# Performance work log

Hardware: AMD Instinct MI355X
Metric: run time of the kernel (lower is better)

## Reference

```python
import jax, jax.numpy as jnp
import numpy as np

N_NODES = 100000
N_EDGES = 3200000
HID = 64


def setup_inputs() -> dict:
    key = jax.random.key(0)
    ks = jax.random.split(key, 20)
    x = jax.random.normal(ks[0], (N_NODES, 3), dtype=jnp.float32)
    edge_index = jax.random.randint(ks[1], (2, N_EDGES), 0, N_NODES, dtype=jnp.int32)

    def glorot(k, fan_in, fan_out):
        s = jnp.sqrt(6.0 / (fan_in + fan_out))
        return jax.random.uniform(k, (fan_in, fan_out), jnp.float32, -s, s)

    W_in = glorot(ks[2], 3, HID)
    b_in = jnp.zeros((HID,), jnp.float32)
    W_hid = jnp.stack([glorot(ks[3 + i], HID, HID) for i in range(6)])  # [6,64,64]
    b_hid = jnp.zeros((6, HID), jnp.float32)
    W_out = glorot(ks[10], HID, 6)
    b_out = jnp.zeros((6,), jnp.float32)
    return {"x": x, "edge_index": edge_index, "W_in": W_in, "b_in": b_in,
            "W_hid": W_hid, "b_hid": b_hid, "W_out": W_out, "b_out": b_out}


def _gcn_layer(x, W, b, src, dst, norm):
    # PyG GCNConv: h = x @ W; out[dst] += norm * h[src]; out += b
    h = x @ W
    msg = h[src] * norm[:, None]            # [E+N, F]
    agg = jax.ops.segment_sum(msg, dst, num_segments=N_NODES)
    return agg + b


def reference(x, edge_index, W_in, b_in, W_hid, b_hid, W_out, b_out):
    # Add self-loops and symmetric normalization (computed once, shared by all layers)
    loops = jnp.arange(N_NODES, dtype=edge_index.dtype)
    src = jnp.concatenate([edge_index[0], loops])
    dst = jnp.concatenate([edge_index[1], loops])
    deg = jax.ops.segment_sum(jnp.ones_like(dst, dtype=x.dtype), dst, num_segments=N_NODES)
    dinv = jnp.where(deg > 0, jax.lax.rsqrt(deg), 0.0)
    norm = dinv[src] * dinv[dst]            # [E+N]

    h = jax.nn.relu(_gcn_layer(x, W_in, b_in, src, dst, norm))
    for i in range(6):
        h = jax.nn.relu(_gcn_layer(h, W_hid[i], b_hid[i], src, dst, norm))
    # dropout p=0.25 with train=False -> identity (eval mode)
    out = _gcn_layer(h, W_out, b_out, src, dst, norm)
    return jax.nn.sigmoid(out)
```

## Files before the change

kernel.cpp:

```cpp
#include <hip/hip_runtime.h>
#include <hip/hip_fp16.h>
#include <math.h>

#define MAXBKT 512


__global__ __launch_bounds__(256) void k_bcount(const int* __restrict__ dstA,
                                                int E, int N, int nbkt, int* bucketCnt) {
    __shared__ int cnt[MAXBKT];
    for (int i = threadIdx.x; i < nbkt; i += 256) cnt[i] = 0;
    __syncthreads();
    int total = E + N;
    for (int i = blockIdx.x * 256 + threadIdx.x; i < total; i += gridDim.x * 256) {
        int d = (i < E) ? dstA[i] : (i - E);
        atomicAdd(&cnt[d >> 8], 1);
    }
    __syncthreads();
    for (int i = threadIdx.x; i < nbkt; i += 256)
        if (cnt[i]) atomicAdd(&bucketCnt[i], cnt[i]);
}

__global__ __launch_bounds__(MAXBKT) void k_bscan(const int* __restrict__ bucketCnt,
                                                  int* bucketOff, int* bucketCur,
                                                  int nbkt, int total) {
    __shared__ int sm[MAXBKT];
    int tid = threadIdx.x;
    int v = (tid < nbkt) ? bucketCnt[tid] : 0;
    sm[tid] = v;
    __syncthreads();
    for (int off = 1; off < MAXBKT; off <<= 1) {
        int t = 0;
        if (tid >= off) t = sm[tid - off];
        __syncthreads();
        sm[tid] += t;
        __syncthreads();
    }
    if (tid < nbkt) {
        int excl = sm[tid] - v;
        bucketOff[tid] = excl;
        bucketCur[tid] = excl;
    }
    if (tid == 0) bucketOff[nbkt] = total;
}

__global__ __launch_bounds__(256) void k_bscat2(const int* __restrict__ srcA,
                                                const int* __restrict__ dstA,
                                                int* bucketCur, unsigned int* bedges,
                                                int E, int N, int nbkt, int chunk) {
    __shared__ int cnt[MAXBKT];
    __shared__ int base[MAXBKT];
    int total = E + N;
    int lo = blockIdx.x * chunk;
    int hi = lo + chunk; if (hi > total) hi = total;
    for (int i = threadIdx.x; i < nbkt; i += 256) cnt[i] = 0;
    __syncthreads();
    for (int i = lo + threadIdx.x; i < hi; i += 256) {
        int d = (i < E) ? dstA[i] : (i - E);
        atomicAdd(&cnt[d >> 8], 1);
    }
    __syncthreads();
    for (int i = threadIdx.x; i < nbkt; i += 256) {
        base[i] = cnt[i] ? atomicAdd(&bucketCur[i], cnt[i]) : 0;
        cnt[i] = 0;
    }
    __syncthreads();
    for (int i = lo + threadIdx.x; i < hi; i += 256) {
        int s, d;
        if (i < E) { s = srcA[i]; d = dstA[i]; }
        else       { s = d = i - E; }
        int b = d >> 8;
        int pos = base[b] + atomicAdd(&cnt[b], 1);
        bedges[pos] = ((unsigned int)(d & 255) << 24) | (unsigned int)s;
    }
}

__global__ __launch_bounds__(256) void k_bfill2(const unsigned int* __restrict__ bedges,
                                                const int* __restrict__ bucketOff,
                                                const float* __restrict__ x,
                                                int* __restrict__ rowptr,
                                                float* __restrict__ dinv,
                                                float* __restrict__ xs,
                                                int* __restrict__ col,
                                                int N, int total) {
    __shared__ int ldeg[256];
    __shared__ int lcur[256];
    int b = blockIdx.x;
    int tid = threadIdx.x;
    int bo = bucketOff[b], be = bucketOff[b + 1];
    ldeg[tid] = 0;
    __syncthreads();
    for (int j = bo + tid; j < be; j += 256)
        atomicAdd(&ldeg[bedges[j] >> 24], 1);
    __syncthreads();
    int dg = ldeg[tid];
    lcur[tid] = dg;
    __syncthreads();
    for (int off = 1; off < 256; off <<= 1) {
        int t = 0;
        if (tid >= off) t = lcur[tid - off];
        __syncthreads();
        lcur[tid] += t;
        __syncthreads();
    }
    int excl = lcur[tid] - dg;
    int node = (b << 8) + tid;
    if (node < N) {
        rowptr[node] = bo + excl;
        float dv = dg > 0 ? rsqrtf((float)dg) : 0.0f;
        dinv[node] = dv;
        xs[node * 3 + 0] = dv * x[node * 3 + 0];
        xs[node * 3 + 1] = dv * x[node * 3 + 1];
        xs[node * 3 + 2] = dv * x[node * 3 + 2];
    }
    if (b == 0 && tid == 0) rowptr[N] = total;
    __syncthreads();
    lcur[tid] = bo + excl;
    __syncthreads();
    for (int j = bo + tid; j < be; j += 256) {
        unsigned int e = bedges[j];
        int pos = atomicAdd(&lcur[e >> 24], 1);
        col[pos] = (int)(e & 0x00FFFFFFu);
    }
}


__global__ __launch_bounds__(256) void k_agg3(const float* __restrict__ xs,
                                              const int* __restrict__ rowptr,
                                              const int* __restrict__ col,
                                              const float* __restrict__ dinv,
                                              float* __restrict__ out3, int n) {
    int i = blockIdx.x * 256 + threadIdx.x;
    if (i >= n) return;
    float a0 = 0.f, a1 = 0.f, a2 = 0.f;
    int beg = rowptr[i], end = rowptr[i + 1];
    for (int j = beg; j < end; ++j) {
        int s = col[j];
        a0 += xs[s * 3 + 0];
        a1 += xs[s * 3 + 1];
        a2 += xs[s * 3 + 2];
    }
    float dv = dinv[i];
    out3[i * 3 + 0] = dv * a0;
    out3[i * 3 + 1] = dv * a1;
    out3[i * 3 + 2] = dv * a2;
}

__global__ __launch_bounds__(256) void k_tin_mm(const float* __restrict__ agg3v,
                                                const float* __restrict__ Win,
                                                const float* __restrict__ bin,
                                                const float* __restrict__ W0,
                                                const float* __restrict__ dinv,
                                                __half* __restrict__ tout, int n) {
    __shared__ float Wl[64 * 64];
    __shared__ float Hl[16][68];
    int tid = threadIdx.x;
    for (int i = tid * 4; i < 4096; i += 1024)
        *(float4*)&Wl[i] = *(const float4*)&W0[i];
    int nodeBase = blockIdx.x * 16;
    {
        int idx = tid * 4;
        int nl = idx >> 6, f0 = idx & 63;
        int node = nodeBase + nl;
        float a0 = 0.f, a1 = 0.f, a2 = 0.f;
        if (node < n) {
            a0 = agg3v[node * 3 + 0];
            a1 = agg3v[node * 3 + 1];
            a2 = agg3v[node * 3 + 2];
        }
        float4 hv;
        float* hp = (float*)&hv;
#pragma unroll
        for (int q = 0; q < 4; ++q) {
            int f = f0 + q;
            float v = bin[f] + a0 * Win[f] + a1 * Win[64 + f] + a2 * Win[128 + f];
            hp[q] = fmaxf(v, 0.f);
        }
        *(float4*)&Hl[nl][f0] = hv;
    }
    __syncthreads();
    int nl = tid >> 4;
    int fq = (tid & 15) * 4;
    float4 acc = make_float4(0.f, 0.f, 0.f, 0.f);
#pragma unroll
    for (int k = 0; k < 64; ++k) {
        float hv = Hl[nl][k];
        float4 wv = *(const float4*)&Wl[k * 64 + fq];
        acc.x += hv * wv.x;
        acc.y += hv * wv.y;
        acc.z += hv * wv.z;
        acc.w += hv * wv.w;
    }
    int node = nodeBase + nl;
    if (node < n) {
        float dv = dinv[node];
        __half2* dst = (__half2*)&tout[(size_t)node * 64 + fq];
        dst[0] = __floats2half2_rn(acc.x * dv, acc.y * dv);
        dst[1] = __floats2half2_rn(acc.z * dv, acc.w * dv);
    }
}

__global__ __launch_bounds__(256) void k_aggmm64(const __half* __restrict__ tin,
                                                 const int* __restrict__ rowptr,
                                                 const int* __restrict__ col,
                                                 const float* __restrict__ dinv,
                                                 const float* __restrict__ bias,
                                                 const float* __restrict__ W,
                                                 __half* __restrict__ tnext, int n) {
    __shared__ float Wl[64 * 64];
    __shared__ float Hl[16][68];
    int tid = threadIdx.x;
    for (int i = tid * 4; i < 4096; i += 1024)
        *(float4*)&Wl[i] = *(const float4*)&W[i];
    int nodeBase = blockIdx.x * 16;
    int wv = tid >> 6;
    int lane = tid & 63;
    int slot = lane >> 3;
    int fl = lane & 7;
#pragma unroll
    for (int k4 = 0; k4 < 4; ++k4) {
        int nl = wv * 4 + k4;
        int node = nodeBase + nl;
        float a0 = 0.f, a1 = 0.f, a2 = 0.f, a3 = 0.f, a4 = 0.f, a5 = 0.f, a6 = 0.f, a7 = 0.f;
        if (node < n) {
            int beg = rowptr[node], end = rowptr[node + 1];
            int j = beg + slot;
            for (; j + 8 < end; j += 16) {
                int s0 = col[j];
                int s1 = col[j + 8];
                float4 r0 = *(const float4*)(tin + (size_t)s0 * 64 + fl * 8);
                float4 r1 = *(const float4*)(tin + (size_t)s1 * 64 + fl * 8);
                const __half2* h0 = (const __half2*)&r0;
                const __half2* h1 = (const __half2*)&r1;
                float2 p;
                p = __half22float2(h0[0]); a0 += p.x; a1 += p.y;
                p = __half22float2(h0[1]); a2 += p.x; a3 += p.y;
                p = __half22float2(h0[2]); a4 += p.x; a5 += p.y;
                p = __half22float2(h0[3]); a6 += p.x; a7 += p.y;
                p = __half22float2(h1[0]); a0 += p.x; a1 += p.y;
                p = __half22float2(h1[1]); a2 += p.x; a3 += p.y;
                p = __half22float2(h1[2]); a4 += p.x; a5 += p.y;
                p = __half22float2(h1[3]); a6 += p.x; a7 += p.y;
            }
            if (j < end) {
                int s0 = col[j];
                float4 r0 = *(const float4*)(tin + (size_t)s0 * 64 + fl * 8);
                const __half2* h0 = (const __half2*)&r0;
                float2 p;
                p = __half22float2(h0[0]); a0 += p.x; a1 += p.y;
                p = __half22float2(h0[1]); a2 += p.x; a3 += p.y;
                p = __half22float2(h0[2]); a4 += p.x; a5 += p.y;
                p = __half22float2(h0[3]); a6 += p.x; a7 += p.y;
            }
        }
#pragma unroll
        for (int m = 8; m < 64; m <<= 1) {
            a0 += __shfl_xor(a0, m, 64);
            a1 += __shfl_xor(a1, m, 64);
            a2 += __shfl_xor(a2, m, 64);
            a3 += __shfl_xor(a3, m, 64);
            a4 += __shfl_xor(a4, m, 64);
            a5 += __shfl_xor(a5, m, 64);
            a6 += __shfl_xor(a6, m, 64);
            a7 += __shfl_xor(a7, m, 64);
        }
        if (slot == 0) {
            float dv = (node < n) ? dinv[node] : 0.f;
            int fo = fl * 8;
            float4 w0, w1;
            w0.x = fmaxf(dv * a0 + bias[fo + 0], 0.f);
            w0.y = fmaxf(dv * a1 + bias[fo + 1], 0.f);
            w0.z = fmaxf(dv * a2 + bias[fo + 2], 0.f);
            w0.w = fmaxf(dv * a3 + bias[fo + 3], 0.f);
            w1.x = fmaxf(dv * a4 + bias[fo + 4], 0.f);
            w1.y = fmaxf(dv * a5 + bias[fo + 5], 0.f);
            w1.z = fmaxf(dv * a6 + bias[fo + 6], 0.f);
            w1.w = fmaxf(dv * a7 + bias[fo + 7], 0.f);
            *(float4*)&Hl[nl][fo] = w0;
            *(float4*)&Hl[nl][fo + 4] = w1;
        }
    }
    __syncthreads();
    int nl = tid >> 4;
    int fq = (tid & 15) * 4;
    float4 acc = make_float4(0.f, 0.f, 0.f, 0.f);
#pragma unroll
    for (int k = 0; k < 64; ++k) {
        float hv = Hl[nl][k];
        float4 wv = *(const float4*)&Wl[k * 64 + fq];
        acc.x += hv * wv.x;
        acc.y += hv * wv.y;
        acc.z += hv * wv.z;
        acc.w += hv * wv.w;
    }
    int node = nodeBase + nl;
    if (node < n) {
        float dv = dinv[node];
        __half2* dst = (__half2*)&tnext[(size_t)node * 64 + fq];
        dst[0] = __floats2half2_rn(acc.x * dv, acc.y * dv);
        dst[1] = __floats2half2_rn(acc.z * dv, acc.w * dv);
    }
}

__global__ __launch_bounds__(256) void k_aggtout(const __half* __restrict__ tin,
                                                 const int* __restrict__ rowptr,
                                                 const int* __restrict__ col,
                                                 const float* __restrict__ dinv,
                                                 const float* __restrict__ bias,
                                                 const float* __restrict__ Wout,
                                                 __half* __restrict__ t6p, int n) {
    __shared__ float Wl6[64 * 6];
    __shared__ float Hl[16][68];
    int tid = threadIdx.x;
    for (int i = tid; i < 384; i += 256) Wl6[i] = Wout[i];
    int nodeBase = blockIdx.x * 16;
    int wv = tid >> 6;
    int lane = tid & 63;
    int slot = lane >> 3;
    int fl = lane & 7;
#pragma unroll
    for (int k4 = 0; k4 < 4; ++k4) {
        int nl = wv * 4 + k4;
        int node = nodeBase + nl;
        float a0 = 0.f, a1 = 0.f, a2 = 0.f, a3 = 0.f, a4 = 0.f, a5 = 0.f, a6 = 0.f, a7 = 0.f;
        if (node < n) {
            int beg = rowptr[node], end = rowptr[node + 1];
            int j = beg + slot;
            for (; j + 8 < end; j += 16) {
                int s0 = col[j];
                int s1 = col[j + 8];
                float4 r0 = *(const float4*)(tin + (size_t)s0 * 64 + fl * 8);
                float4 r1 = *(const float4*)(tin + (size_t)s1 * 64 + fl * 8);
                const __half2* h0 = (const __half2*)&r0;
                const __half2* h1 = (const __half2*)&r1;
                float2 p;
                p = __half22float2(h0[0]); a0 += p.x; a1 += p.y;
                p = __half22float2(h0[1]); a2 += p.x; a3 += p.y;
                p = __half22float2(h0[2]); a4 += p.x; a5 += p.y;
                p = __half22float2(h0[3]); a6 += p.x; a7 += p.y;
                p = __half22float2(h1[0]); a0 += p.x; a1 += p.y;
                p = __half22float2(h1[1]); a2 += p.x; a3 += p.y;
                p = __half22float2(h1[2]); a4 += p.x; a5 += p.y;
                p = __half22float2(h1[3]); a6 += p.x; a7 += p.y;
            }
            if (j < end) {
                int s0 = col[j];
                float4 r0 = *(const float4*)(tin + (size_t)s0 * 64 + fl * 8);
                const __half2* h0 = (const __half2*)&r0;
                float2 p;
                p = __half22float2(h0[0]); a0 += p.x; a1 += p.y;
                p = __half22float2(h0[1]); a2 += p.x; a3 += p.y;
                p = __half22float2(h0[2]); a4 += p.x; a5 += p.y;
                p = __half22float2(h0[3]); a6 += p.x; a7 += p.y;
            }
        }
#pragma unroll
        for (int m = 8; m < 64; m <<= 1) {
            a0 += __shfl_xor(a0, m, 64);
            a1 += __shfl_xor(a1, m, 64);
            a2 += __shfl_xor(a2, m, 64);
            a3 += __shfl_xor(a3, m, 64);
            a4 += __shfl_xor(a4, m, 64);
            a5 += __shfl_xor(a5, m, 64);
            a6 += __shfl_xor(a6, m, 64);
            a7 += __shfl_xor(a7, m, 64);
        }
        if (slot == 0) {
            float dv = (node < n) ? dinv[node] : 0.f;
            int fo = fl * 8;
            float4 w0, w1;
            w0.x = fmaxf(dv * a0 + bias[fo + 0], 0.f);
            w0.y = fmaxf(dv * a1 + bias[fo + 1], 0.f);
            w0.z = fmaxf(dv * a2 + bias[fo + 2], 0.f);
            w0.w = fmaxf(dv * a3 + bias[fo + 3], 0.f);
            w1.x = fmaxf(dv * a4 + bias[fo + 4], 0.f);
            w1.y = fmaxf(dv * a5 + bias[fo + 5], 0.f);
            w1.z = fmaxf(dv * a6 + bias[fo + 6], 0.f);
            w1.w = fmaxf(dv * a7 + bias[fo + 7], 0.f);
            *(float4*)&Hl[nl][fo] = w0;
            *(float4*)&Hl[nl][fo + 4] = w1;
        }
    }
    __syncthreads();
    int nl = tid >> 4;
    int f = tid & 15;
    int node = nodeBase + nl;
    if (node < n && f < 8) {
        __half o = __float2half(0.f);
        if (f < 6) {
            float acc = 0.f;
#pragma unroll
            for (int k = 0; k < 64; ++k) acc += Hl[nl][k] * Wl6[k * 6 + f];
            o = __float2half(dinv[node] * acc);
        }
        t6p[(size_t)node * 8 + f] = o;
    }
}

__global__ __launch_bounds__(256) void k_agg6(const __half* __restrict__ t6p,
                                              const int* __restrict__ rowptr,
                                              const int* __restrict__ col,
                                              const float* __restrict__ dinv,
                                              const float* __restrict__ bout,
                                              float* __restrict__ out, int n) {
    int i = blockIdx.x * 256 + threadIdx.x;
    if (i >= n) return;
    float a0 = 0.f, a1 = 0.f, a2 = 0.f, a3 = 0.f, a4 = 0.f, a5 = 0.f;
    int beg = rowptr[i], end = rowptr[i + 1];
    int j = beg;
    for (; j + 1 < end; j += 2) {
        int s0 = col[j], s1 = col[j + 1];
        float4 r0 = *(const float4*)(t6p + (size_t)s0 * 8);
        float4 r1 = *(const float4*)(t6p + (size_t)s1 * 8);
        const __half2* h0 = (const __half2*)&r0;
        const __half2* h1 = (const __half2*)&r1;
        float2 p;
        p = __half22float2(h0[0]); a0 += p.x; a1 += p.y;
        p = __half22float2(h0[1]); a2 += p.x; a3 += p.y;
        p = __half22float2(h0[2]); a4 += p.x; a5 += p.y;
        p = __half22float2(h1[0]); a0 += p.x; a1 += p.y;
        p = __half22float2(h1[1]); a2 += p.x; a3 += p.y;
        p = __half22float2(h1[2]); a4 += p.x; a5 += p.y;
    }
    if (j < end) {
        int s0 = col[j];
        float4 r0 = *(const float4*)(t6p + (size_t)s0 * 8);
        const __half2* h0 = (const __half2*)&r0;
        float2 p;
        p = __half22float2(h0[0]); a0 += p.x; a1 += p.y;
        p = __half22float2(h0[1]); a2 += p.x; a3 += p.y;
        p = __half22float2(h0[2]); a4 += p.x; a5 += p.y;
    }
    float dv = dinv[i];
    out[i * 6 + 0] = 1.0f / (1.0f + expf(-(dv * a0 + bout[0])));
    out[i * 6 + 1] = 1.0f / (1.0f + expf(-(dv * a1 + bout[1])));
    out[i * 6 + 2] = 1.0f / (1.0f + expf(-(dv * a2 + bout[2])));
    out[i * 6 + 3] = 1.0f / (1.0f + expf(-(dv * a3 + bout[3])));
    out[i * 6 + 4] = 1.0f / (1.0f + expf(-(dv * a4 + bout[4])));
    out[i * 6 + 5] = 1.0f / (1.0f + expf(-(dv * a5 + bout[5])));
}


extern "C" void kernel_launch(void* const* d_in, const int* in_sizes, int n_in,
                              void* d_out, int out_size, void* d_ws, size_t ws_size,
                              hipStream_t stream) {
    const float* x    = (const float*)d_in[0];
    const int*   eidx = (const int*)d_in[1];
    const float* Win  = (const float*)d_in[2];
    const float* bin  = (const float*)d_in[3];
    const float* Whid = (const float*)d_in[4];
    const float* bhid = (const float*)d_in[5];
    const float* Wout = (const float*)d_in[6];
    const float* bout = (const float*)d_in[7];
    float* out = (float*)d_out;

    const int N = in_sizes[0] / 3;
    const int E = in_sizes[1] / 2;
    const int* srcA = eidx;
    const int* dstA = eidx + E;
    const int TOT = E + N;
    const int NBKT = (N + 255) >> 8;

    char* p = (char*)d_ws;
    auto alloc = [&](size_t bytes) -> void* {
        void* r = (void*)p;
        p += (bytes + 255) & ~(size_t)255;
        return r;
    };
    float*        dinv      = (float*)alloc((size_t)N * 4);
    int*          rowptr    = (int*)alloc((size_t)(N + 1) * 4);
    int*          bucketCnt = (int*)alloc((size_t)MAXBKT * 4);
    int*          bucketOff = (int*)alloc((size_t)(MAXBKT + 1) * 4);
    int*          bucketCur = (int*)alloc((size_t)MAXBKT * 4);
    unsigned int* bedges    = (unsigned int*)alloc((size_t)TOT * 4);
    int*          col       = (int*)alloc((size_t)TOT * 4);
    float*        xs        = (float*)alloc((size_t)N * 3 * 4);
    float*        agg3buf   = (float*)alloc((size_t)N * 3 * 4);
    __half*       tA        = (__half*)alloc((size_t)N * 64 * 2);
    __half*       tB        = (__half*)alloc((size_t)N * 64 * 2);
    __half*       t6p       = (__half*)alloc((size_t)N * 8 * 2);

    const int NB_N = (N + 255) / 256;
    const int NB16 = (N + 15) / 16;

    hipMemsetAsync(bucketCnt, 0, (size_t)MAXBKT * 4, stream);
    k_bcount<<<512, 256, 0, stream>>>(dstA, E, N, NBKT, bucketCnt);
    k_bscan<<<1, MAXBKT, 0, stream>>>(bucketCnt, bucketOff, bucketCur, NBKT, TOT);
    const int CHUNK = (TOT + 511) / 512;
    k_bscat2<<<512, 256, 0, stream>>>(srcA, dstA, bucketCur, bedges, E, N, NBKT, CHUNK);
    k_bfill2<<<NBKT, 256, 0, stream>>>(bedges, bucketOff, x, rowptr, dinv, xs, col, N, TOT);

    k_agg3<<<NB_N, 256, 0, stream>>>(xs, rowptr, col, dinv, agg3buf, N);
    k_tin_mm<<<NB16, 256, 0, stream>>>(agg3buf, Win, bin, Whid, dinv, tA, N);

    __half* tin = tA;
    __half* tnx = tB;
    for (int i = 1; i <= 5; ++i) {
        k_aggmm64<<<NB16, 256, 0, stream>>>(tin, rowptr, col, dinv,
                                            bhid + (size_t)(i - 1) * 64,
                                            Whid + (size_t)i * 4096, tnx, N);
        __half* tmp = tin; tin = tnx; tnx = tmp;
    }

    k_aggtout<<<NB16, 256, 0, stream>>>(tin, rowptr, col, dinv,
                                        bhid + (size_t)5 * 64, Wout, t6p, N);

    k_agg6<<<NB_N, 256, 0, stream>>>(t6p, rowptr, col, dinv, bout, out, N);
}
```

Baseline: 683.3 us.

## Assign one wavefront per node with 512-thread blocks and deeper gather unroll

The fused aggregate+matmul kernels now use 512-thread blocks covering 8 nodes. Each wavefront handles a single node instead of looping over four nodes in sequence, and the neighbor gather loop is unrolled to four outstanding 16-byte loads per lane. The small matmul is changed to one output feature per thread with scalar half stores. The aim is more memory-level parallelism and less serialization in the latency-bound gather, at the cost of more blocks that each reload the 16KB weight tile into LDS, so weight-load overhead per node doubles.

```diff
diff --git a/kernel.cpp b/kernel.cpp
--- a/kernel.cpp
+++ b/kernel.cpp
@@ -145,61 +145,40 @@
     out3[i * 3 + 2] = dv * a2;
 }
 
-__global__ __launch_bounds__(256) void k_tin_mm(const float* __restrict__ agg3v,
+__global__ __launch_bounds__(512) void k_tin_mm(const float* __restrict__ agg3v,
                                                 const float* __restrict__ Win,
                                                 const float* __restrict__ bin,
                                                 const float* __restrict__ W0,
                                                 const float* __restrict__ dinv,
                                                 __half* __restrict__ tout, int n) {
     __shared__ float Wl[64 * 64];
-    __shared__ float Hl[16][68];
+    __shared__ float Hl[8][68];
     int tid = threadIdx.x;
-    for (int i = tid * 4; i < 4096; i += 1024)
+    {
+        int i = tid * 4;
         *(float4*)&Wl[i] = *(const float4*)&W0[i];
-    int nodeBase = blockIdx.x * 16;
-    {
-        int idx = tid * 4;
-        int nl = idx >> 6, f0 = idx & 63;
-        int node = nodeBase + nl;
-        float a0 = 0.f, a1 = 0.f, a2 = 0.f;
-        if (node < n) {
-            a0 = agg3v[node * 3 + 0];
-            a1 = agg3v[node * 3 + 1];
-            a2 = agg3v[node * 3 + 2];
-        }
-        float4 hv;
-        float* hp = (float*)&hv;
-#pragma unroll
-        for (int q = 0; q < 4; ++q) {
-            int f = f0 + q;
-            float v = bin[f] + a0 * Win[f] + a1 * Win[64 + f] + a2 * Win[128 + f];
-            hp[q] = fmaxf(v, 0.f);
-        }
-        *(float4*)&Hl[nl][f0] = hv;
-    }
-    __syncthreads();
-    int nl = tid >> 4;
-    int fq = (tid & 15) * 4;
-    float4 acc = make_float4(0.f, 0.f, 0.f, 0.f);
-#pragma unroll
-    for (int k = 0; k < 64; ++k) {
-        float hv = Hl[nl][k];
-        float4 wv = *(const float4*)&Wl[k * 64 + fq];
-        acc.x += hv * wv.x;
-        acc.y += hv * wv.y;
-        acc.z += hv * wv.z;
-        acc.w += hv * wv.w;
-    }
+        *(float4*)&Wl[i + 2048] = *(const float4*)&W0[i + 2048];
+    }
+    int nodeBase = blockIdx.x * 8;
+    int nl = tid >> 6, f = tid & 63;
     int node = nodeBase + nl;
     if (node < n) {
-        float dv = dinv[node];
-        __half2* dst = (__half2*)&tout[(size_t)node * 64 + fq];
-        dst[0] = __floats2half2_rn(acc.x * dv, acc.y * dv);
-        dst[1] = __floats2half2_rn(acc.z * dv, acc.w * dv);
-    }
-}
-
-__global__ __launch_bounds__(256) void k_aggmm64(const __half* __restrict__ tin,
+        float a0 = agg3v[node * 3 + 0];
+        float a1 = agg3v[node * 3 + 1];
+        float a2 = agg3v[node * 3 + 2];
+        float v = bin[f] + a0 * Win[f] + a1 * Win[64 + f] + a2 * Win[128 + f];
+        Hl[nl][f] = fmaxf(v, 0.f);
+    }
+    __syncthreads();
+    if (node < n) {
+        float acc = 0.f;
+#pragma unroll
+        for (int k = 0; k < 64; ++k) acc += Hl[nl][k] * Wl[k * 64 + f];
+        tout[(size_t)node * 64 + f] = __float2half(acc * dinv[node]);
+    }
+}
+
+__global__ __launch_bounds__(512) void k_aggmm64(const __half* __restrict__ tin,
                                                  const int* __restrict__ rowptr,
                                                  const int* __restrict__ col,
                                                  const float* __restrict__ dinv,
@@ -207,101 +186,99 @@
                                                  const float* __restrict__ W,
                                                  __half* __restrict__ tnext, int n) {
     __shared__ float Wl[64 * 64];
-    __shared__ float Hl[16][68];
+    __shared__ float Hl[8][68];
     int tid = threadIdx.x;
-    for (int i = tid * 4; i < 4096; i += 1024)
+    {
+        int i = tid * 4;
         *(float4*)&Wl[i] = *(const float4*)&W[i];
-    int nodeBase = blockIdx.x * 16;
+        *(float4*)&Wl[i + 2048] = *(const float4*)&W[i + 2048];
+    }
+    int nodeBase = blockIdx.x * 8;
     int wv = tid >> 6;
     int lane = tid & 63;
     int slot = lane >> 3;
     int fl = lane & 7;
+    int node = nodeBase + wv;
+    float a0 = 0.f, a1 = 0.f, a2 = 0.f, a3 = 0.f, a4 = 0.f, a5 = 0.f, a6 = 0.f, a7 = 0.f;
+    if (node < n) {
+        int beg = rowptr[node], end = rowptr[node + 1];
+        int j = beg + slot;
+        for (; j + 24 < end; j += 32) {
+            int s0 = col[j], s1 = col[j + 8], s2 = col[j + 16], s3 = col[j + 24];
+            float4 r0 = *(const float4*)(tin + (size_t)s0 * 64 + fl * 8);
+            float4 r1 = *(const float4*)(tin + (size_t)s1 * 64 + fl * 8);
+            float4 r2 = *(const float4*)(tin + (size_t)s2 * 64 + fl * 8);
+            float4 r3 = *(const float4*)(tin + (size_t)s3 * 64 + fl * 8);
+            const __half2* h0 = (const __half2*)&r0;
+            const __half2* h1 = (const __half2*)&r1;
+            const __half2* h2 = (const __half2*)&r2;
+            const __half2* h3 = (const __half2*)&r3;
+            float2 p;
+            p = __half22float2(h0[0]); a0 += p.x; a1 += p.y;
+            p = __half22float2(h0[1]); a2 += p.x; a3 += p.y;
+            p = __half22float2(h0[2]); a4 += p.x; a5 += p.y;
+            p = __half22float2(h0[3]); a6 += p.x; a7 += p.y;
+            p = __half22float2(h1[0]); a0 += p.x; a1 += p.y;
+            p = __half22float2(h1[1]); a2 += p.x; a3 += p.y;
+            p = __half22float2(h1[2]); a4 += p.x; a5 += p.y;
+            p = __half22float2(h1[3]); a6 += p.x; a7 += p.y;
+            p = __half22float2(h2[0]); a0 += p.x; a1 += p.y;
+            p = __half22float2(h2[1]); a2 += p.x; a3 += p.y;
+            p = __half22float2(h2[2]); a4 += p.x; a5 += p.y;
+            p = __half22float2(h2[3]); a6 += p.x; a7 += p.y;
+            p = __half22float2(h3[0]); a0 += p.x; a1 += p.y;
+            p = __half22float2(h3[1]); a2 += p.x; a3 += p.y;
+            p = __half22float2(h3[2]); a4 += p.x; a5 += p.y;
+            p = __half22float2(h3[3]); a6 += p.x; a7 += p.y;
+        }
+        for (; j < end; j += 8) {
+            int s0 = col[j];
+            float4 r0 = *(const float4*)(tin + (size_t)s0 * 64 + fl * 8);
+            const __half2* h0 = (const __half2*)&r0;
+            float2 p;
+            p = __half22float2(h0[0]); a0 += p.x; a1 += p.y;
+            p = __half22float2(h0[1]); a2 += p.x; a3 += p.y;
+            p = __half22float2(h0[2]); a4 += p.x; a5 += p.y;
+            p = __half22float2(h0[3]); a6 += p.x; a7 += p.y;
+        }
+    }
 #pragma unroll
-    for (int k4 = 0; k4 < 4; ++k4) {
-        int nl = wv * 4 + k4;
-        int node = nodeBase + nl;
-        float a0 = 0.f, a1 = 0.f, a2 = 0.f, a3 = 0.f, a4 = 0.f, a5 = 0.f, a6 = 0.f, a7 = 0.f;
-        if (node < n) {
-            int beg = rowptr[node], end = rowptr[node + 1];
-            int j = beg + slot;
-            for (; j + 8 < end; j += 16) {
-                int s0 = col[j];
-                int s1 = col[j + 8];
-                float4 r0 = *(const float4*)(tin + (size_t)s0 * 64 + fl * 8);
-                float4 r1 = *(const float4*)(tin + (size_t)s1 * 64 + fl * 8);
-                const __half2* h0 = (const __half2*)&r0;
-                const __half2* h1 = (const __half2*)&r1;
-                float2 p;
-                p = __half22float2(h0[0]); a0 += p.x; a1 += p.y;
-                p = __half22float2(h0[1]); a2 += p.x; a3 += p.y;
-                p = __half22float2(h0[2]); a4 += p.x; a5 += p.y;
-                p = __half22float2(h0[3]); a6 += p.x; a7 += p.y;
-                p = __half22float2(h1[0]); a0 += p.x; a1 += p.y;
-                p = __half22float2(h1[1]); a2 += p.x; a3 += p.y;
-                p = __half22float2(h1[2]); a4 += p.x; a5 += p.y;
-                p = __half22float2(h1[3]); a6 += p.x; a7 += p.y;
-            }
-            if (j < end) {
-                int s0 = col[j];
-                float4 r0 = *(const float4*)(tin + (size_t)s0 * 64 + fl * 8);
-                const __half2* h0 = (const __half2*)&r0;
-                float2 p;
-                p = __half22float2(h0[0]); a0 += p.x; a1 += p.y;
-                p = __half22float2(h0[1]); a2 += p.x; a3 += p.y;
-                p = __half22float2(h0[2]); a4 += p.x; a5 += p.y;
-                p = __half22float2(h0[3]); a6 += p.x; a7 += p.y;
-            }
-        }
+    for (int m = 8; m < 64; m <<= 1) {
+        a0 += __shfl_xor(a0, m, 64);
+        a1 += __shfl_xor(a1, m, 64);
+        a2 += __shfl_xor(a2, m, 64);
+        a3 += __shfl_xor(a3, m, 64);
+        a4 += __shfl_xor(a4, m, 64);
+        a5 += __shfl_xor(a5, m, 64);
+        a6 += __shfl_xor(a6, m, 64);
+        a7 += __shfl_xor(a7, m, 64);
+    }
+    if (slot == 0 && node < n) {
+        float dv = dinv[node];
+        int fo = fl * 8;
+        float4 w0, w1;
+        w0.x = fmaxf(dv * a0 + bias[fo + 0], 0.f);
+        w0.y = fmaxf(dv * a1 + bias[fo + 1], 0.f);
+        w0.z = fmaxf(dv * a2 + bias[fo + 2], 0.f);
+        w0.w = fmaxf(dv * a3 + bias[fo + 3], 0.f);
+        w1.x = fmaxf(dv * a4 + bias[fo + 4], 0.f);
+        w1.y = fmaxf(dv * a5 + bias[fo + 5], 0.f);
+        w1.z = fmaxf(dv * a6 + bias[fo + 6], 0.f);
+        w1.w = fmaxf(dv * a7 + bias[fo + 7], 0.f);
+        *(float4*)&Hl[wv][fo] = w0;
+        *(float4*)&Hl[wv][fo + 4] = w1;
+    }
+    __syncthreads();
+    if (node < n) {
+        int f = lane;
+        float acc = 0.f;
 #pragma unroll
-        for (int m = 8; m < 64; m <<= 1) {
-            a0 += __shfl_xor(a0, m, 64);
-            a1 += __shfl_xor(a1, m, 64);
-            a2 += __shfl_xor(a2, m, 64);
-            a3 += __shfl_xor(a3, m, 64);
-            a4 += __shfl_xor(a4, m, 64);
-            a5 += __shfl_xor(a5, m, 64);
-            a6 += __shfl_xor(a6, m, 64);
-            a7 += __shfl_xor(a7, m, 64);
-        }
-        if (slot == 0) {
-            float dv = (node < n) ? dinv[node] : 0.f;
-            int fo = fl * 8;
-            float4 w0, w1;
-            w0.x = fmaxf(dv * a0 + bias[fo + 0], 0.f);
-            w0.y = fmaxf(dv * a1 + bias[fo + 1], 0.f);
-            w0.z = fmaxf(dv * a2 + bias[fo + 2], 0.f);
-            w0.w = fmaxf(dv * a3 + bias[fo + 3], 0.f);
-            w1.x = fmaxf(dv * a4 + bias[fo + 4], 0.f);
-            w1.y = fmaxf(dv * a5 + bias[fo + 5], 0.f);
-            w1.z = fmaxf(dv * a6 + bias[fo + 6], 0.f);
-            w1.w = fmaxf(dv * a7 + bias[fo + 7], 0.f);
-            *(float4*)&Hl[nl][fo] = w0;
-            *(float4*)&Hl[nl][fo + 4] = w1;
-        }
-    }
-    __syncthreads();
-    int nl = tid >> 4;
-    int fq = (tid & 15) * 4;
-    float4 acc = make_float4(0.f, 0.f, 0.f, 0.f);
-#pragma unroll
-    for (int k = 0; k < 64; ++k) {
-        float hv = Hl[nl][k];
-        float4 wv = *(const float4*)&Wl[k * 64 + fq];
-        acc.x += hv * wv.x;
-        acc.y += hv * wv.y;
-        acc.z += hv * wv.z;
-        acc.w += hv * wv.w;
-    }
-    int node = nodeBase + nl;
-    if (node < n) {
-        float dv = dinv[node];
-        __half2* dst = (__half2*)&tnext[(size_t)node * 64 + fq];
-        dst[0] = __floats2half2_rn(acc.x * dv, acc.y * dv);
-        dst[1] = __floats2half2_rn(acc.z * dv, acc.w * dv);
-    }
-}
-
-__global__ __launch_bounds__(256) void k_aggtout(const __half* __restrict__ tin,
+        for (int k = 0; k < 64; ++k) acc += Hl[wv][k] * Wl[k * 64 + f];
+        tnext[(size_t)node * 64 + f] = __float2half(acc * dinv[node]);
+    }
+}
+
+__global__ __launch_bounds__(512) void k_aggtout(const __half* __restrict__ tin,
                                                  const int* __restrict__ rowptr,
                                                  const int* __restrict__ col,
                                                  const float* __restrict__ dinv,
@@ -309,90 +286,94 @@
                                                  const float* __restrict__ Wout,
                                                  __half* __restrict__ t6p, int n) {
     __shared__ float Wl6[64 * 6];
-    __shared__ float Hl[16][68];
+    __shared__ float Hl[8][68];
     int tid = threadIdx.x;
-    for (int i = tid; i < 384; i += 256) Wl6[i] = Wout[i];
-    int nodeBase = blockIdx.x * 16;
+    if (tid < 384) Wl6[tid] = Wout[tid];
+    int nodeBase = blockIdx.x * 8;
     int wv = tid >> 6;
     int lane = tid & 63;
     int slot = lane >> 3;
     int fl = lane & 7;
+    int node = nodeBase + wv;
+    float a0 = 0.f, a1 = 0.f, a2 = 0.f, a3 = 0.f, a4 = 0.f, a5 = 0.f, a6 = 0.f, a7 = 0.f;
+    if (node < n) {
+        int beg = rowptr[node], end = rowptr[node + 1];
+        int j = beg + slot;
+        for (; j + 24 < end; j += 32) {
+            int s0 = col[j], s1 = col[j + 8], s2 = col[j + 16], s3 = col[j + 24];
+            float4 r0 = *(const float4*)(tin + (size_t)s0 * 64 + fl * 8);
+            float4 r1 = *(const float4*)(tin + (size_t)s1 * 64 + fl * 8);
+            float4 r2 = *(const float4*)(tin + (size_t)s2 * 64 + fl * 8);
+            float4 r3 = *(const float4*)(tin + (size_t)s3 * 64 + fl * 8);
+            const __half2* h0 = (const __half2*)&r0;
+            const __half2* h1 = (const __half2*)&r1;
+            const __half2* h2 = (const __half2*)&r2;
+            const __half2* h3 = (const __half2*)&r3;
+            float2 p;
+            p = __half22float2(h0[0]); a0 += p.x; a1 += p.y;
+            p = __half22float2(h0[1]); a2 += p.x; a3 += p.y;
+            p = __half22float2(h0[2]); a4 += p.x; a5 += p.y;
+            p = __half22float2(h0[3]); a6 += p.x; a7 += p.y;
+            p = __half22float2(h1[0]); a0 += p.x; a1 += p.y;
+            p = __half22float2(h1[1]); a2 += p.x; a3 += p.y;
+            p = __half22float2(h1[2]); a4 += p.x; a5 += p.y;
+            p = __half22float2(h1[3]); a6 += p.x; a7 += p.y;
+            p = __half22float2(h2[0]); a0 += p.x; a1 += p.y;
+            p = __half22float2(h2[1]); a2 += p.x; a3 += p.y;
+            p = __half22float2(h2[2]); a4 += p.x; a5 += p.y;
+            p = __half22float2(h2[3]); a6 += p.x; a7 += p.y;
+            p = __half22float2(h3[0]); a0 += p.x; a1 += p.y;
+            p = __half22float2(h3[1]); a2 += p.x; a3 += p.y;
+            p = __half22float2(h3[2]); a4 += p.x; a5 += p.y;
+            p = __half22float2(h3[3]); a6 += p.x; a7 += p.y;
+        }
+        for (; j < end; j += 8) {
+            int s0 = col[j];
+            float4 r0 = *(const float4*)(tin + (size_t)s0 * 64 + fl * 8);
+            const __half2* h0 = (const __half2*)&r0;
+            float2 p;
+            p = __half22float2(h0[0]); a0 += p.x; a1 += p.y;
+            p = __half22float2(h0[1]); a2 += p.x; a3 += p.y;
+            p = __half22float2(h0[2]); a4 += p.x; a5 += p.y;
+            p = __half22float2(h0[3]); a6 += p.x; a7 += p.y;
+        }
+    }
 #pragma unroll
-    for (int k4 = 0; k4 < 4; ++k4) {
-        int nl = wv * 4 + k4;
-        int node = nodeBase + nl;
-        float a0 = 0.f, a1 = 0.f, a2 = 0.f, a3 = 0.f, a4 = 0.f, a5 = 0.f, a6 = 0.f, a7 = 0.f;
-        if (node < n) {
-            int beg = rowptr[node], end = rowptr[node + 1];
-            int j = beg + slot;
-            for (; j + 8 < end; j += 16) {
-                int s0 = col[j];
-                int s1 = col[j + 8];
-                float4 r0 = *(const float4*)(tin + (size_t)s0 * 64 + fl * 8);
-                float4 r1 = *(const float4*)(tin + (size_t)s1 * 64 + fl * 8);
-                const __half2* h0 = (const __half2*)&r0;
-                const __half2* h1 = (const __half2*)&r1;
-                float2 p;
-                p = __half22float2(h0[0]); a0 += p.x; a1 += p.y;
-                p = __half22float2(h0[1]); a2 += p.x; a3 += p.y;
-                p = __half22float2(h0[2]); a4 += p.x; a5 += p.y;
-                p = __half22float2(h0[3]); a6 += p.x; a7 += p.y;
-                p = __half22float2(h1[0]); a0 += p.x; a1 += p.y;
-                p = __half22float2(h1[1]); a2 += p.x; a3 += p.y;
-                p = __half22float2(h1[2]); a4 += p.x; a5 += p.y;
-                p = __half22float2(h1[3]); a6 += p.x; a7 += p.y;
-            }
-            if (j < end) {
-                int s0 = col[j];
-                float4 r0 = *(const float4*)(tin + (size_t)s0 * 64 + fl * 8);
-                const __half2* h0 = (const __half2*)&r0;
-                float2 p;
-                p = __half22float2(h0[0]); a0 += p.x; a1 += p.y;
-                p = __half22float2(h0[1]); a2 += p.x; a3 += p.y;
-                p = __half22float2(h0[2]); a4 += p.x; a5 += p.y;
-                p = __half22float2(h0[3]); a6 += p.x; a7 += p.y;
-            }
-        }
-#pragma unroll
-        for (int m = 8; m < 64; m <<= 1) {
-            a0 += __shfl_xor(a0, m, 64);
-            a1 += __shfl_xor(a1, m, 64);
-            a2 += __shfl_xor(a2, m, 64);
-            a3 += __shfl_xor(a3, m, 64);
-            a4 += __shfl_xor(a4, m, 64);
-            a5 += __shfl_xor(a5, m, 64);
-            a6 += __shfl_xor(a6, m, 64);
-            a7 += __shfl_xor(a7, m, 64);
-        }
-        if (slot == 0) {
-            float dv = (node < n) ? dinv[node] : 0.f;
-            int fo = fl * 8;
-            float4 w0, w1;
-            w0.x = fmaxf(dv * a0 + bias[fo + 0], 0.f);
-            w0.y = fmaxf(dv * a1 + bias[fo + 1], 0.f);
-            w0.z = fmaxf(dv * a2 + bias[fo + 2], 0.f);
-            w0.w = fmaxf(dv * a3 + bias[fo + 3], 0.f);
-            w1.x = fmaxf(dv * a4 + bias[fo + 4], 0.f);
-            w1.y = fmaxf(dv * a5 + bias[fo + 5], 0.f);
-            w1.z = fmaxf(dv * a6 + bias[fo + 6], 0.f);
-            w1.w = fmaxf(dv * a7 + bias[fo + 7], 0.f);
-            *(float4*)&Hl[nl][fo] = w0;
-            *(float4*)&Hl[nl][fo + 4] = w1;
-        }
-    }
-    __syncthreads();
-    int nl = tid >> 4;
-    int f = tid & 15;
-    int node = nodeBase + nl;
-    if (node < n && f < 8) {
+    for (int m = 8; m < 64; m <<= 1) {
+        a0 += __shfl_xor(a0, m, 64);
+        a1 += __shfl_xor(a1, m, 64);
+        a2 += __shfl_xor(a2, m, 64);
+        a3 += __shfl_xor(a3, m, 64);
+        a4 += __shfl_xor(a4, m, 64);
+        a5 += __shfl_xor(a5, m, 64);
+        a6 += __shfl_xor(a6, m, 64);
+        a7 += __shfl_xor(a7, m, 64);
+    }
+    if (slot == 0 && node < n) {
+        float dv = dinv[node];
+        int fo = fl * 8;
+        float4 w0, w1;
+        w0.x = fmaxf(dv * a0 + bias[fo + 0], 0.f);
+        w0.y = fmaxf(dv * a1 + bias[fo + 1], 0.f);
+        w0.z = fmaxf(dv * a2 + bias[fo + 2], 0.f);
+        w0.w = fmaxf(dv * a3 + bias[fo + 3], 0.f);
+        w1.x = fmaxf(dv * a4 + bias[fo + 4], 0.f);
+        w1.y = fmaxf(dv * a5 + bias[fo + 5], 0.f);
+        w1.z = fmaxf(dv * a6 + bias[fo + 6], 0.f);
+        w1.w = fmaxf(dv * a7 + bias[fo + 7], 0.f);
+        *(float4*)&Hl[wv][fo] = w0;
+        *(float4*)&Hl[wv][fo + 4] = w1;
+    }
+    __syncthreads();
+    if (node < n && lane < 8) {
         __half o = __float2half(0.f);
-        if (f < 6) {
+        if (lane < 6) {
             float acc = 0.f;
 #pragma unroll
-            for (int k = 0; k < 64; ++k) acc += Hl[nl][k] * Wl6[k * 6 + f];
-            o = __float2half(dinv[node] * acc);
+            for (int k = 0; k < 64; ++k) acc += Hl[wv][k] * Wl6[k * 6 + lane];
+            o = __float2half(acc * dinv[node]);
         }
-        t6p[(size_t)node * 8 + f] = o;
+        t6p[(size_t)node * 8 + lane] = o;
     }
 }
 
@@ -480,7 +461,7 @@
     __half*       t6p       = (__half*)alloc((size_t)N * 8 * 2);
 
     const int NB_N = (N + 255) / 256;
-    const int NB16 = (N + 15) / 16;
+    const int NB8  = (N + 7) / 8;
 
     hipMemsetAsync(bucketCnt, 0, (size_t)MAXBKT * 4, stream);
     k_bcount<<<512, 256, 0, stream>>>(dstA, E, N, NBKT, bucketCnt);
@@ -490,19 +471,19 @@
     k_bfill2<<<NBKT, 256, 0, stream>>>(bedges, bucketOff, x, rowptr, dinv, xs, col, N, TOT);
 
     k_agg3<<<NB_N, 256, 0, stream>>>(xs, rowptr, col, dinv, agg3buf, N);
-    k_tin_mm<<<NB16, 256, 0, stream>>>(agg3buf, Win, bin, Whid, dinv, tA, N);
+    k_tin_mm<<<NB8, 512, 0, stream>>>(agg3buf, Win, bin, Whid, dinv, tA, N);
 
     __half* tin = tA;
     __half* tnx = tB;
     for (int i = 1; i <= 5; ++i) {
-        k_aggmm64<<<NB16, 256, 0, stream>>>(tin, rowptr, col, dinv,
-                                            bhid + (size_t)(i - 1) * 64,
-                                            Whid + (size_t)i * 4096, tnx, N);
+        k_aggmm64<<<NB8, 512, 0, stream>>>(tin, rowptr, col, dinv,
+                                           bhid + (size_t)(i - 1) * 64,
+                                           Whid + (size_t)i * 4096, tnx, N);
         __half* tmp = tin; tin = tnx; tnx = tmp;
     }
 
-    k_aggtout<<<NB16, 256, 0, stream>>>(tin, rowptr, col, dinv,
-                                        bhid + (size_t)5 * 64, Wout, t6p, N);
+    k_aggtout<<<NB8, 512, 0, stream>>>(tin, rowptr, col, dinv,
+                                       bhid + (size_t)5 * 64, Wout, t6p, N);
 
     k_agg6<<<NB_N, 256, 0, stream>>>(t6p, rowptr, col, dinv, bout, out, N);
 }
```

Result: slower. 770.5 us (+12.8%).
